# Kernel tuning notes

Hardware: AMD Instinct MI355X
Metric: run time of the kernel (lower is better)

The kernel has to match this reference:

```python
import jax, jax.numpy as jnp
import numpy as np

EMBED_DIM = 2048
NUM_HEADS = 16
HEAD_DIM = EMBED_DIM // NUM_HEADS


def setup_inputs() -> dict:
    key = jax.random.key(0)
    k_x, k_qkv, k_out = jax.random.split(key, 3)
    x = jax.random.normal(k_x, (4, 2048, EMBED_DIM), dtype=jnp.float32)
    # torch nn.Linear(in, out) weight is [out, in]; y = x @ W.T
    scale = 1.0 / np.sqrt(EMBED_DIM)
    W_qkv = jax.random.uniform(k_qkv, (3 * EMBED_DIM, EMBED_DIM), dtype=jnp.float32, minval=-scale, maxval=scale)
    W_out = jax.random.uniform(k_out, (EMBED_DIM, EMBED_DIM), dtype=jnp.float32, minval=-scale, maxval=scale)
    return {"x": x, "W_qkv": W_qkv, "W_out": W_out}


def reference(x, W_qkv, W_out):
    B, T, C = x.shape
    H, D = NUM_HEADS, HEAD_DIM
    qkv = jnp.einsum("btc,fc->btf", x, W_qkv)  # [B,T,3C]
    q, k, v = jnp.split(qkv, 3, axis=-1)
    q = q.reshape(B, T, H, D).transpose(0, 2, 1, 3)  # [B,H,T,D]
    k = k.reshape(B, T, H, D).transpose(0, 2, 1, 3)
    v = v.reshape(B, T, H, D).transpose(0, 2, 1, 3)
    att = jnp.einsum("bhqd,bhkd->bhqk", q, k) / jnp.sqrt(jnp.float32(D))
    causal = jnp.tril(jnp.ones((T, T), dtype=bool))
    att = jnp.where(causal[None, None], att, -jnp.inf)
    att = jax.nn.softmax(att, axis=-1)
    out = jnp.einsum("bhqk,bhkd->bhqd", att, v)  # [B,H,T,D]
    out = out.transpose(0, 2, 1, 3).reshape(B, T, C)
    return jnp.einsum("btc,oc->bto", out, W_out)
```

## Files before the change

kernel.cpp:

```cpp
#include <hip/hip_runtime.h>
#include <hip/hip_bf16.h>
#include <math.h>

#define BDIM 4
#define TDIM 2048
#define CDIM 2048
#define HDIM 16
#define DDIM 128
#define MROWS (BDIM*TDIM)
#define NQKV (3*CDIM)
#define GK   CDIM
#define QSZ  (MROWS*CDIM)

#define NTILES 32
#define NITER  16
#define HT     8192
#define BOFF   32768

#define QSCALE 0.1275171f

typedef __attribute__((ext_vector_type(8))) short short8;
typedef __attribute__((ext_vector_type(4))) unsigned short ushort4v;
typedef __attribute__((ext_vector_type(4))) float f32x4;
typedef __attribute__((ext_vector_type(16))) float f32x16;

__device__ __forceinline__ unsigned short f2bf(float f) {
    unsigned int u = __float_as_uint(f);
    u += 0x7fffu + ((u >> 16) & 1u);
    return (unsigned short)(u >> 16);
}

__device__ __forceinline__ unsigned int cvtpk_bf16(float lo, float hi) {
    unsigned int r;
    asm("v_cvt_pk_bf16_f32 %0, %1, %2" : "=v"(r) : "v"(lo), "v"(hi));
    return r;
}

__device__ __forceinline__ void gload16(const unsigned short* g, unsigned short* l) {
    __builtin_amdgcn_global_load_lds((__attribute__((address_space(1))) void*)(g),
                                     (__attribute__((address_space(3))) void*)(l),
                                     16, 0, 0);
}

__global__ __launch_bounds__(256) void cvt_all(const float* __restrict__ x,
                                               const float* __restrict__ wqkv,
                                               const float* __restrict__ wout,
                                               unsigned short* __restrict__ xb,
                                               unsigned short* __restrict__ wqkvb,
                                               unsigned short* __restrict__ woutb)
{
    const int stride = gridDim.x * blockDim.x;
    const int t0 = blockIdx.x * blockDim.x + threadIdx.x;
    for (int i = t0; i < MROWS*CDIM/4; i += stride) {
        float4 f = ((const float4*)x)[i];
        ushort4v u;
        u[0]=f2bf(f.x); u[1]=f2bf(f.y); u[2]=f2bf(f.z); u[3]=f2bf(f.w);
        ((ushort4v*)xb)[i] = u;
    }
    for (int i = t0; i < NQKV*CDIM/4; i += stride) {
        float4 f = ((const float4*)wqkv)[i];
        const float s = (i < CDIM*CDIM/4) ? QSCALE : 1.0f;
        ushort4v u;
        u[0]=f2bf(f.x*s); u[1]=f2bf(f.y*s); u[2]=f2bf(f.z*s); u[3]=f2bf(f.w*s);
        ((ushort4v*)wqkvb)[i] = u;
    }
    for (int i = t0; i < CDIM*CDIM/4; i += stride) {
        float4 f = ((const float4*)wout)[i];
        ushort4v u;
        u[0]=f2bf(f.x); u[1]=f2bf(f.y); u[2]=f2bf(f.z); u[3]=f2bf(f.w);
        ((ushort4v*)woutb)[i] = u;
    }
}

__device__ __forceinline__ void stage_half(const unsigned short* __restrict__ T,
                                           int rowbase, int kcol,
                                           unsigned short* dst, int w, int lane)
{
    const int sw = ((lane & 3) ^ ((lane >> 3) & 3)) * 8;
#pragma unroll
    for (int j = 0; j < 2; ++j) {
        const int r = w*32 + j*16 + (lane >> 2);
        gload16(T + (size_t)(rowbase + r)*GK + kcol + sw, dst + (w*32 + j*16)*32);
    }
}

template<int MQ, int KS, int BUF, bool RDB, int WN>
__device__ __forceinline__ void gphase(unsigned short* lds,
    const unsigned short* __restrict__ stT, int stRow, int stKcol, unsigned short* stDst,
    int wr, int wc, int fr, int colu, int w, int lane,
    short8 (&bfr)[4], f32x4 (&acc)[8][4])
{
    const unsigned short* Ah = lds + (BUF*2 + KS)*HT;
    const unsigned short* Bh = lds + BOFF + (BUF*2 + KS)*HT;
    short8 af[4];
#pragma unroll
    for (int mi = 0; mi < 4; ++mi)
        af[mi] = *(const short8*)&Ah[(wr*128 + (MQ*4 + mi)*16 + fr)*32 + colu];
    if (RDB) {
#pragma unroll
        for (int nj = 0; nj < 4; ++nj)
            bfr[nj] = *(const short8*)&Bh[(wc*64 + nj*16 + fr)*32 + colu];
    }
    stage_half(stT, stRow, stKcol, stDst, w, lane);
    if (WN == 8) asm volatile("s_waitcnt vmcnt(8)" ::: "memory");
    __builtin_amdgcn_s_barrier();
    asm volatile("s_waitcnt lgkmcnt(0)" ::: "memory");
    __builtin_amdgcn_sched_barrier(0);
    __builtin_amdgcn_s_setprio(1);
#pragma unroll
    for (int mi = 0; mi < 4; ++mi)
#pragma unroll
        for (int nj = 0; nj < 4; ++nj)
            acc[MQ*4 + mi][nj] = __builtin_amdgcn_mfma_f32_16x16x32_bf16(af[mi], bfr[nj], acc[MQ*4 + mi][nj], 0, 0, 0);
    __builtin_amdgcn_s_setprio(0);
    __builtin_amdgcn_s_barrier();
}

template<int MODE, int RX>
__global__ __launch_bounds__(512, 2) void gemm8(const unsigned short* __restrict__ A,
                                                const unsigned short* __restrict__ B,
                                                float* __restrict__ outp,
                                                unsigned short* __restrict__ qb,
                                                unsigned short* __restrict__ kb,
                                                unsigned short* __restrict__ vt,
                                                int Nsz)
{
    extern __shared__ unsigned short lds[];
    const int tid  = threadIdx.x;
    const int w    = tid >> 6;
    const int lane = tid & 63;
    const int wr   = w >> 2, wc = w & 3;
    const int fr   = lane & 15;
    const int fg   = lane >> 4;
    const int colu = (fg ^ ((fr >> 1) & 3)) * 8;

    const int gx  = gridDim.x, gy = gridDim.y;
    const int id  = blockIdx.x + blockIdx.y * gx;
    const int xcd = id & 7;
    const int jj  = id >> 3;
    const int mx  = gx / RX;
    const int my  = (gy * RX) >> 3;
    const int bx  = (xcd % RX) * mx + (jj % mx);
    const int by  = (xcd / RX) * my + (jj / mx);
    const int m0  = bx * 256, n0 = by * 256;

    f32x4 acc[8][4];
#pragma unroll
    for (int i = 0; i < 8; ++i)
#pragma unroll
        for (int j = 0; j < 4; ++j) acc[i][j] = (f32x4)(0.f);
    short8 bfr[4];

    stage_half(A, m0, 0,  lds,             w, lane);
    stage_half(B, n0, 0,  lds + BOFF,      w, lane);
    stage_half(A, m0, 32, lds + HT,        w, lane);
    stage_half(B, n0, 32, lds + BOFF + HT, w, lane);
    stage_half(A, m0, 64, lds + 2*HT,        w, lane);
    stage_half(B, n0, 64, lds + BOFF + 2*HT, w, lane);
    asm volatile("s_waitcnt vmcnt(0)" ::: "memory");
    __builtin_amdgcn_s_barrier();

    for (int i = 0; i < NITER; ++i) {
        const int t1 = 2*i + 1;
        const int t2 = (2*i + 2 < NTILES) ? 2*i + 2 : 0;
        const int t3 = (2*i + 3 < NTILES) ? 2*i + 3 : 0;
        gphase<0,0,0,true ,0>(lds, A, m0, t1*64+32, lds + 3*HT,        wr, wc, fr, colu, w, lane, bfr, acc);
        gphase<1,0,0,false,8>(lds, B, n0, t1*64+32, lds + BOFF + 3*HT, wr, wc, fr, colu, w, lane, bfr, acc);
        gphase<0,1,0,true ,0>(lds, A, m0, t2*64,    lds,               wr, wc, fr, colu, w, lane, bfr, acc);
        gphase<1,1,0,false,8>(lds, B, n0, t2*64,    lds + BOFF,        wr, wc, fr, colu, w, lane, bfr, acc);
        gphase<0,0,1,true ,0>(lds, A, m0, t2*64+32, lds + HT,          wr, wc, fr, colu, w, lane, bfr, acc);
        gphase<1,0,1,false,8>(lds, B, n0, t2*64+32, lds + BOFF + HT,   wr, wc, fr, colu, w, lane, bfr, acc);
        gphase<0,1,1,true ,0>(lds, A, m0, t3*64,    lds + 2*HT,        wr, wc, fr, colu, w, lane, bfr, acc);
        gphase<1,1,1,false,8>(lds, B, n0, t3*64,    lds + BOFF + 2*HT, wr, wc, fr, colu, w, lane, bfr, acc);
    }
    asm volatile("s_waitcnt vmcnt(0)" ::: "memory");

    if (MODE == 0) {
#pragma unroll
        for (int mi = 0; mi < 8; ++mi)
#pragma unroll
            for (int nj = 0; nj < 4; ++nj) {
                const int n   = n0 + wc*64 + nj*16 + fr;
                const int sel = n >> 11;
                const int c   = n & 2047;
                const int hh  = c >> 7, dd = c & 127;
                const int mb  = m0 + wr*128 + mi*16 + fg*4;
                const int bb  = mb >> 11, tt = mb & 2047;
                if (sel == 2) {
                    ushort4v v;
#pragma unroll
                    for (int r = 0; r < 4; ++r) v[r] = f2bf(acc[mi][nj][r]);
                    *(ushort4v*)&vt[((size_t)(bb*HDIM + hh)*DDIM + dd)*TDIM + tt] = v;
                } else {
                    unsigned short* dstb = (sel == 0) ? qb : kb;
#pragma unroll
                    for (int r = 0; r < 4; ++r)
                        dstb[((size_t)(bb*HDIM + hh)*TDIM + tt + r)*DDIM + dd] = f2bf(acc[mi][nj][r]);
                }
            }
    } else {
#pragma unroll
        for (int mi = 0; mi < 8; ++mi)
#pragma unroll
            for (int nj = 0; nj < 4; ++nj) {
                const int n = n0 + wc*64 + nj*16 + fr;
#pragma unroll
                for (int r = 0; r < 4; ++r) {
                    const int m = m0 + wr*128 + mi*16 + fg*4 + r;
                    outp[(size_t)m*Nsz + n] = acc[mi][nj][r];
                }
            }
    }
}

__global__ __launch_bounds__(512) void attn_mfma(const unsigned short* __restrict__ Qg,
                                                 const unsigned short* __restrict__ Kg,
                                                 const unsigned short* __restrict__ Vt,
                                                 unsigned short* __restrict__ attb)
{
    extern __shared__ unsigned short smem[];
    unsigned short* KsB = smem;
    unsigned short* VsB = smem + 16384;

    const int tid  = threadIdx.x;
    const int w    = tid >> 6;
    const int lane = tid & 63;
    const int lq   = lane & 31;
    const int hi   = lane >> 5;
    const int bh   = blockIdx.x & 63;
    const int qb_  = 7 - (blockIdx.x >> 6);
    const int q0   = qb_ * 256;
    const int qt   = 4*qb_ + 3;
    const int qw   = q0 + w*32;

    const unsigned short* Kbh  = Kg + (size_t)bh*TDIM*DDIM;
    const unsigned short* Vtbh = Vt + (size_t)bh*DDIM*TDIM;

    short8 qf[8];
    {
        const unsigned short* qrow = Qg + ((size_t)bh*TDIM + qw + lq)*DDIM + hi*8;
#pragma unroll
        for (int ds = 0; ds < 8; ++ds)
            qf[ds] = *(const short8*)(qrow + ds*16);
    }

    f32x16 oacc[4];
#pragma unroll
    for (int i = 0; i < 4; ++i) oacc[i] = (f32x16)(0.f);
    float m_r = -INFINITY, l_r = 0.f;

#define STAGE_K(buf, kt_)                                                        \
    {                                                                            \
        _Pragma("unroll")                                                        \
        for (int j = 0; j < 2; ++j) {                                            \
            const int rw  = (w<<3) + (j<<2) + (lane >> 4);                       \
            const int sub = (lane & 15) ^ (rw & 15);                             \
            gload16(Kbh + ((size_t)((kt_)*64 + rw))*DDIM + sub*8,                \
                    &KsB[(buf)*8192 + ((w<<3) + (j<<2))*128]);                   \
        }                                                                        \
    }
#define STAGE_V(buf, kt_)                                                        \
    {                                                                            \
        _Pragma("unroll")                                                        \
        for (int j = 0; j < 2; ++j) {                                            \
            const int d   = (w<<4) + (j<<3) + (lane >> 3);                       \
            const int sub = (lane & 7) ^ (d & 7);                                \
            gload16(Vtbh + (size_t)d*TDIM + (kt_)*64 + sub*8,                    \
                    &VsB[(buf)*8192 + ((w<<4) + (j<<3))*64]);                    \
        }                                                                        \
    }

    STAGE_K(0, 0);
    STAGE_V(0, 0);
    __syncthreads();

    for (int kt = 0; kt <= qt; ++kt) {
        const int cur = kt & 1;
        if (kt < qt) { STAGE_K(cur ^ 1, kt + 1); STAGE_V(cur ^ 1, kt + 1); }

#pragma unroll
        for (int ks2 = 0; ks2 < 2; ++ks2) {
            const int ktb = kt*64 + ks2*32;
            if (ktb <= qw + 31) {
                f32x16 sa = (f32x16)(0.f);
#pragma unroll
                for (int ds = 0; ds < 8; ++ds) {
                    const int kvl = ks2*32 + lq;
                    short8 kf = *(const short8*)&KsB[cur*8192 +
                        ((kvl*128 + ds*16 + hi*8) ^ ((kvl & 15) << 3))];
                    sa = __builtin_amdgcn_mfma_f32_32x32x16_bf16(kf, qf[ds], sa, 0, 0, 0);
                }

                if (ktb + 31 > qw) {
#pragma unroll
                    for (int r = 0; r < 16; ++r) {
                        const int kvg = ktb + (r&3) + 8*(r>>2) + 4*hi;
                        if (kvg > qw + lq) sa[r] = -INFINITY;
                    }
                }

                float p[16];
                bool slow = (kt == 0) && (ks2 == 0);
                if (!slow) {
                    float pm = 0.f;
#pragma unroll
                    for (int r = 0; r < 16; ++r) {
                        p[r] = exp2f(sa[r] - m_r);
                        pm = fmaxf(pm, p[r]);
                    }
                    slow = __any(pm > 256.0f);
                }
                if (slow) {
                    float mx = sa[0];
#pragma unroll
                    for (int r = 1; r < 16; ++r) mx = fmaxf(mx, sa[r]);
                    mx = fmaxf(mx, __shfl_xor(mx, 32));
                    const float mn = fmaxf(m_r, mx);
                    const float corr = exp2f(m_r - mn);
                    m_r = mn;
#pragma unroll
                    for (int r = 0; r < 16; ++r) p[r] = exp2f(sa[r] - m_r);
                    l_r *= corr;
#pragma unroll
                    for (int r = 0; r < 16; ++r) {
                        const float cr = __shfl(corr, (r&3) + 8*(r>>2) + 4*hi);
#pragma unroll
                        for (int dt = 0; dt < 4; ++dt) oacc[dt][r] *= cr;
                    }
                }

                float ls = 0.f;
#pragma unroll
                for (int r = 0; r < 16; ++r) ls += p[r];
                l_r += ls + __shfl_xor(ls, 32);

                short8 pa[2];
#pragma unroll
                for (int ks = 0; ks < 2; ++ks) {
                    const unsigned int wA = cvtpk_bf16(p[8*ks+0], p[8*ks+1]);
                    const unsigned int wB = cvtpk_bf16(p[8*ks+2], p[8*ks+3]);
                    const unsigned int wC = cvtpk_bf16(p[8*ks+4], p[8*ks+5]);
                    const unsigned int wD = cvtpk_bf16(p[8*ks+6], p[8*ks+7]);
                    const unsigned int u = __shfl_xor(hi ? wA : wC, 32);
                    const unsigned int v = __shfl_xor(hi ? wB : wD, 32);
                    unsigned int a0 = hi ? u  : wA;
                    unsigned int a1 = hi ? v  : wB;
                    unsigned int a2 = hi ? wC : u;
                    unsigned int a3 = hi ? wD : v;
                    unsigned int aw[4] = {a0, a1, a2, a3};
                    pa[ks] = *(short8*)aw;
                }

#pragma unroll
                for (int ks = 0; ks < 2; ++ks)
#pragma unroll
                    for (int dt = 0; dt < 4; ++dt) {
                        const int d = dt*32 + lq;
                        short8 vf = *(const short8*)&VsB[cur*8192 +
                            ((d*64 + ks2*32 + ks*16 + hi*8) ^ ((d & 7) << 3))];
                        oacc[dt] = __builtin_amdgcn_mfma_f32_32x32x16_bf16(pa[ks], vf, oacc[dt], 0, 0, 0);
                    }
            }
        }

        __syncthreads();
    }

    const float inv = 1.f / l_r;
    const int b = bh >> 4, h = bh & 15;
#pragma unroll
    for (int r = 0; r < 16; ++r) {
        const int qrw = (r&3) + 8*(r>>2) + 4*hi;
        const float invq = __shfl(inv, qrw);
        unsigned short* obase = attb + ((size_t)b*TDIM + qw + qrw)*CDIM + h*DDIM + lq;
#pragma unroll
        for (int dt = 0; dt < 4; ++dt)
            obase[dt*32] = f2bf(oacc[dt][r] * invq);
    }
}

extern "C" void kernel_launch(void* const* d_in, const int* in_sizes, int n_in,
                              void* d_out, int out_size, void* d_ws, size_t ws_size,
                              hipStream_t stream)
{
    const float* x    = (const float*)d_in[0];
    const float* Wqkv = (const float*)d_in[1];
    const float* Wout = (const float*)d_in[2];
    float* out = (float*)d_out;

    unsigned short* ws = (unsigned short*)d_ws;
    unsigned short* xb    = ws;
    unsigned short* Wqkvb = xb    + (size_t)MROWS*CDIM;
    unsigned short* Woutb = Wqkvb + (size_t)NQKV*CDIM;
    unsigned short* Qb    = Woutb + (size_t)CDIM*CDIM;
    unsigned short* Kb    = Qb + QSZ;
    unsigned short* Vtb   = Kb + QSZ;
    unsigned short* attb  = Vtb + QSZ;

    cvt_all<<<2048, 256, 0, stream>>>(x, Wqkv, Wout, xb, Wqkvb, Woutb);
    gemm8<0,4><<<dim3(MROWS/256, NQKV/256), 512, 131072, stream>>>(xb, Wqkvb, nullptr, Qb, Kb, Vtb, NQKV);
    attn_mfma<<<dim3(64*8), 512, 65536, stream>>>(Qb, Kb, Vtb, attb);
    gemm8<1,2><<<dim3(MROWS/256, CDIM/256), 512, 131072, stream>>>(attb, Woutb, out, nullptr, nullptr, nullptr, CDIM);
}
```

Before: 395.0 us.

## Merge GEMM half-phases into full-tile phases with 4-deep LDS pipeline

```diff
diff --git a/kernel.cpp b/kernel.cpp
--- a/kernel.cpp
+++ b/kernel.cpp
@@ -84,34 +84,34 @@
     }
 }
 
-template<int MQ, int KS, int BUF, bool RDB, int WN>
-__device__ __forceinline__ void gphase(unsigned short* lds,
-    const unsigned short* __restrict__ stT, int stRow, int stKcol, unsigned short* stDst,
+template<int RD, int SR>
+__device__ __forceinline__ void gphase4(unsigned short* lds,
+    const unsigned short* __restrict__ A, const unsigned short* __restrict__ B,
+    int m0, int n0, int kcol,
     int wr, int wc, int fr, int colu, int w, int lane,
-    short8 (&bfr)[4], f32x4 (&acc)[8][4])
-{
-    const unsigned short* Ah = lds + (BUF*2 + KS)*HT;
-    const unsigned short* Bh = lds + BOFF + (BUF*2 + KS)*HT;
-    short8 af[4];
-#pragma unroll
-    for (int mi = 0; mi < 4; ++mi)
-        af[mi] = *(const short8*)&Ah[(wr*128 + (MQ*4 + mi)*16 + fr)*32 + colu];
-    if (RDB) {
-#pragma unroll
-        for (int nj = 0; nj < 4; ++nj)
-            bfr[nj] = *(const short8*)&Bh[(wc*64 + nj*16 + fr)*32 + colu];
-    }
-    stage_half(stT, stRow, stKcol, stDst, w, lane);
-    if (WN == 8) asm volatile("s_waitcnt vmcnt(8)" ::: "memory");
+    f32x4 (&acc)[8][4])
+{
+    const unsigned short* Ah = lds + RD*HT;
+    const unsigned short* Bh = lds + BOFF + RD*HT;
+    short8 af[8], bfr[4];
+#pragma unroll
+    for (int mi = 0; mi < 8; ++mi)
+        af[mi] = *(const short8*)&Ah[(wr*128 + mi*16 + fr)*32 + colu];
+#pragma unroll
+    for (int nj = 0; nj < 4; ++nj)
+        bfr[nj] = *(const short8*)&Bh[(wc*64 + nj*16 + fr)*32 + colu];
+    stage_half(A, m0, kcol, lds + SR*HT, w, lane);
+    stage_half(B, n0, kcol, lds + BOFF + SR*HT, w, lane);
+    asm volatile("s_waitcnt vmcnt(8)" ::: "memory");
     __builtin_amdgcn_s_barrier();
     asm volatile("s_waitcnt lgkmcnt(0)" ::: "memory");
     __builtin_amdgcn_sched_barrier(0);
     __builtin_amdgcn_s_setprio(1);
 #pragma unroll
-    for (int mi = 0; mi < 4; ++mi)
+    for (int mi = 0; mi < 8; ++mi)
 #pragma unroll
         for (int nj = 0; nj < 4; ++nj)
-            acc[MQ*4 + mi][nj] = __builtin_amdgcn_mfma_f32_16x16x32_bf16(af[mi], bfr[nj], acc[MQ*4 + mi][nj], 0, 0, 0);
+            acc[mi][nj] = __builtin_amdgcn_mfma_f32_16x16x32_bf16(af[mi], bfr[nj], acc[mi][nj], 0, 0, 0);
     __builtin_amdgcn_s_setprio(0);
     __builtin_amdgcn_s_barrier();
 }
@@ -149,7 +149,6 @@
     for (int i = 0; i < 8; ++i)
 #pragma unroll
         for (int j = 0; j < 4; ++j) acc[i][j] = (f32x4)(0.f);
-    short8 bfr[4];
 
     stage_half(A, m0, 0,  lds,             w, lane);
     stage_half(B, n0, 0,  lds + BOFF,      w, lane);
@@ -157,21 +156,17 @@
     stage_half(B, n0, 32, lds + BOFF + HT, w, lane);
     stage_half(A, m0, 64, lds + 2*HT,        w, lane);
     stage_half(B, n0, 64, lds + BOFF + 2*HT, w, lane);
-    asm volatile("s_waitcnt vmcnt(0)" ::: "memory");
+    asm volatile("s_waitcnt vmcnt(8)" ::: "memory");
     __builtin_amdgcn_s_barrier();
 
     for (int i = 0; i < NITER; ++i) {
         const int t1 = 2*i + 1;
         const int t2 = (2*i + 2 < NTILES) ? 2*i + 2 : 0;
         const int t3 = (2*i + 3 < NTILES) ? 2*i + 3 : 0;
-        gphase<0,0,0,true ,0>(lds, A, m0, t1*64+32, lds + 3*HT,        wr, wc, fr, colu, w, lane, bfr, acc);
-        gphase<1,0,0,false,8>(lds, B, n0, t1*64+32, lds + BOFF + 3*HT, wr, wc, fr, colu, w, lane, bfr, acc);
-        gphase<0,1,0,true ,0>(lds, A, m0, t2*64,    lds,               wr, wc, fr, colu, w, lane, bfr, acc);
-        gphase<1,1,0,false,8>(lds, B, n0, t2*64,    lds + BOFF,        wr, wc, fr, colu, w, lane, bfr, acc);
-        gphase<0,0,1,true ,0>(lds, A, m0, t2*64+32, lds + HT,          wr, wc, fr, colu, w, lane, bfr, acc);
-        gphase<1,0,1,false,8>(lds, B, n0, t2*64+32, lds + BOFF + HT,   wr, wc, fr, colu, w, lane, bfr, acc);
-        gphase<0,1,1,true ,0>(lds, A, m0, t3*64,    lds + 2*HT,        wr, wc, fr, colu, w, lane, bfr, acc);
-        gphase<1,1,1,false,8>(lds, B, n0, t3*64,    lds + BOFF + 2*HT, wr, wc, fr, colu, w, lane, bfr, acc);
+        gphase4<0,3>(lds, A, B, m0, n0, t1*64+32, wr, wc, fr, colu, w, lane, acc);
+        gphase4<1,0>(lds, A, B, m0, n0, t2*64,    wr, wc, fr, colu, w, lane, acc);
+        gphase4<2,1>(lds, A, B, m0, n0, t2*64+32, wr, wc, fr, colu, w, lane, acc);
+        gphase4<3,2>(lds, A, B, m0, n0, t3*64,    wr, wc, fr, colu, w, lane, acc);
     }
     asm volatile("s_waitcnt vmcnt(0)" ::: "memory");
 
@@ -302,12 +297,13 @@
                 float p[16];
                 bool slow = (kt == 0) && (ks2 == 0);
                 if (!slow) {
-                    float pm = 0.f;
 #pragma unroll
                     for (int r = 0; r < 16; ++r) {
                         p[r] = exp2f(sa[r] - m_r);
-                        pm = fmaxf(pm, p[r]);
                     }
+                    float pm = p[0];
+#pragma unroll
+                    for (int r = 1; r < 16; ++r) pm = fmaxf(pm, p[r]);
                     slow = __any(pm > 256.0f);
                 }
                 if (slow) {
```

Measured after the change: 396.1 us. About the same (+0.3%).
